# Performance work log

Measured on AMD Instinct MI355X. Metric: run time of the kernel, lower is better.

Reference implementation:

```python
import jax, jax.numpy as jnp
import numpy as np

NUM_HEADS = 16   # matches init_kwargs
WARP_Q = 32      # per-warp Q quant granularity (rows)
BLK_K = 64       # per-block K quant granularity (rows)
EPS = 1e-8


def setup_inputs() -> dict:
    key = jax.random.key(0)
    kq, kk, kv = jax.random.split(key, 3)
    b, s, hid = 2, 2048, 2048
    q = jax.random.normal(kq, (b, s, hid), jnp.float32)
    k = jax.random.normal(kk, (b, s, hid), jnp.float32)
    v = jax.random.normal(kv, (b, s, hid), jnp.float32)
    return {"q": q, "k": k, "v": v, "window_left": 1024, "window_right": 1024}


def _quant_int8(x, group):
    # x: [b, h, s, d] -> int8-valued floats + per-row scales [b, h, s, 1]
    b, h, s, d = x.shape
    xg = x.reshape(b, h, s // group, group, d)
    scale = jnp.maximum(jnp.max(jnp.abs(xg), axis=(3, 4), keepdims=True) / 127.0, EPS)
    xq = jnp.clip(jnp.round(xg / scale), -127.0, 127.0)
    scale_rows = jnp.broadcast_to(scale, (b, h, s // group, group, 1)).reshape(b, h, s, 1)
    return xq.reshape(b, h, s, d), scale_rows


def _sage_attention(q, k, v, window_left, window_right):
    b, s, hid = q.shape
    n = NUM_HEADS
    d = hid // n
    sm_scale = 1.0 / np.sqrt(d)
    # [b, s, n*d] -> [b, n, s, d]
    qh = q.reshape(b, s, n, d).transpose(0, 2, 1, 3)
    kh = k.reshape(b, s, n, d).transpose(0, 2, 1, 3)
    vh = v.reshape(b, s, n, d).transpose(0, 2, 1, 3)

    # smooth K: subtract per-channel seq mean (softmax-invariant)
    k_mean = jnp.mean(kh, axis=2, keepdims=True)
    ks = kh - k_mean

    # per-warp int8 quantization of Q and K
    qq, q_scale = _quant_int8(qh, WARP_Q)
    kq, k_scale = _quant_int8(ks, BLK_K)

    # int8 QK^T, dequantized: [b, n, s, s]
    scores = jnp.einsum('bhid,bhjd->bhij', qq, kq)
    scores = scores * q_scale * jnp.swapaxes(k_scale, -1, -2) * sm_scale

    # sliding window mask (window < 0 means unlimited on that side)
    i = jnp.arange(s)[:, None]
    j = jnp.arange(s)[None, :]
    allowed = jnp.ones((s, s), dtype=bool)
    if window_left >= 0:
        allowed = allowed & ((i - j) <= window_left)
    if window_right >= 0:
        allowed = allowed & ((j - i) <= window_right)
    scores = jnp.where(allowed, scores, -jnp.inf)

    p = jax.nn.softmax(scores, axis=-1)

    # smooth V + fp16 PV accumulation
    v_mean = jnp.mean(vh, axis=2, keepdims=True)
    out16 = jnp.matmul(p.astype(jnp.float16), (vh - v_mean).astype(jnp.float16),
                       preferred_element_type=jnp.float16)
    out = out16.astype(jnp.float32) + v_mean  # rows of p sum to 1

    # [b, n, s, d] -> [b, s, n*d]
    return out.transpose(0, 2, 1, 3).reshape(b, s, n * d)


def reference(q, k, v, window_left, window_right):
    return _sage_attention(q, k, v, window_left, window_right)
```

## Files before the change

### kernel.cpp

```cpp
#include <hip/hip_runtime.h>
#include <hip/hip_fp16.h>
#include <math.h>

#define S_LEN 2048
#define NHID  2048
#define D_HEAD 128
#define N_BH  32
#define EPS_Q 1e-8f

typedef _Float16 half8 __attribute__((ext_vector_type(8)));
typedef _Float16 half4 __attribute__((ext_vector_type(4)));
typedef float floatx4 __attribute__((ext_vector_type(4)));
typedef int int4v __attribute__((ext_vector_type(4)));

__global__ void means_kernel(const float* __restrict__ kk, const float* __restrict__ vv,
                             float* __restrict__ ksumP, float* __restrict__ vsumP) {
  int blk = blockIdx.x;
  int bh = blk >> 5, chunk = blk & 31;
  int b = bh >> 4, h = bh & 15;
  int t = threadIdx.x;
  int d4 = t & 31, sg = t >> 5;
  int s0 = chunk * 64;
  const long base = ((long)(b * S_LEN + s0)) * NHID + h * D_HEAD + d4 * 4;
  floatx4 ks = {0.f,0.f,0.f,0.f}, vs = {0.f,0.f,0.f,0.f};
  #pragma unroll
  for (int j = 0; j < 8; ++j) {
    long idx = base + (long)(sg * 8 + j) * NHID;
    ks += *(const floatx4*)(kk + idx);
    vs += *(const floatx4*)(vv + idx);
  }
  __shared__ floatx4 red[256];
  red[t] = ks; __syncthreads();
  if (t < 128) red[t] += red[t + 128]; __syncthreads();
  if (t < 64)  red[t] += red[t + 64];  __syncthreads();
  if (t < 32) *(floatx4*)(ksumP + (long)blk * 128 + t * 4) = red[t] + red[t + 32];
  __syncthreads();
  red[t] = vs; __syncthreads();
  if (t < 128) red[t] += red[t + 128]; __syncthreads();
  if (t < 64)  red[t] += red[t + 64];  __syncthreads();
  if (t < 32) *(floatx4*)(vsumP + (long)blk * 128 + t * 4) = red[t] + red[t + 32];
}

__global__ void prep_kernel(const float* __restrict__ q, const float* __restrict__ k,
                            const float* __restrict__ v,
                            const float* __restrict__ ksumP, const float* __restrict__ vsumP,
                            signed char* __restrict__ qq, signed char* __restrict__ kq,
                            _Float16* __restrict__ vt,
                            float* __restrict__ qscale, float* __restrict__ kscale,
                            float* __restrict__ vmean) {
  int blk = blockIdx.x;
  int t = threadIdx.x;
  int lane = t & 63, wid = t >> 6;
  __shared__ float wred[4];
  __shared__ __align__(16) _Float16 tile[64 * 136];
  int d4 = t & 31, sg = t >> 5;

  if (blk < 2048) {
    int bh = blk >> 6, g = blk & 63;
    int b = bh >> 4, h = bh & 15;
    int s0 = g * 32;
    const long gbase = ((long)(b * S_LEN + s0)) * NHID + h * D_HEAD + d4 * 4;
    floatx4 vals[4]; float am = 0.f;
    #pragma unroll
    for (int j = 0; j < 4; ++j) {
      floatx4 x = *(const floatx4*)(q + gbase + (long)(sg + j * 8) * NHID);
      vals[j] = x;
      am = fmaxf(am, fmaxf(fmaxf(fabsf(x[0]), fabsf(x[1])), fmaxf(fabsf(x[2]), fabsf(x[3]))));
    }
    #pragma unroll
    for (int off = 1; off < 64; off <<= 1) am = fmaxf(am, __shfl_xor(am, off, 64));
    if (lane == 0) wred[wid] = am;
    __syncthreads();
    am = fmaxf(fmaxf(wred[0], wred[1]), fmaxf(wred[2], wred[3]));
    float scale = fmaxf(am / 127.0f, EPS_Q);
    if (t == 0) qscale[bh * 64 + g] = scale;
    float inv = 1.0f / scale;
    #pragma unroll
    for (int j = 0; j < 4; ++j) {
      int pk = 0;
      #pragma unroll
      for (int c = 0; c < 4; ++c) {
        int qv = (int)fminf(fmaxf(rintf(vals[j][c] * inv), -127.f), 127.f);
        pk |= (qv & 255) << (8 * c);
      }
      ((int*)qq)[((long)bh * S_LEN + s0 + sg + j * 8) * 32 + d4] = pk;
    }
  } else if (blk < 3072) {
    int bb = blk - 2048;
    int bh = bb >> 5, g = bb & 31;
    int b = bh >> 4, h = bh & 15;
    int s0 = g * 64;
    floatx4 msum = {0.f,0.f,0.f,0.f};
    #pragma unroll
    for (int c = 0; c < 32; ++c)
      msum += *(const floatx4*)(ksumP + (long)(bh * 32 + c) * 128 + d4 * 4);
    floatx4 mean = msum * (1.0f / 2048.0f);
    const long gbase = ((long)(b * S_LEN + s0)) * NHID + h * D_HEAD + d4 * 4;
    floatx4 vals[8]; float am = 0.f;
    #pragma unroll
    for (int j = 0; j < 8; ++j) {
      floatx4 x = *(const floatx4*)(k + gbase + (long)(sg + j * 8) * NHID) - mean;
      vals[j] = x;
      am = fmaxf(am, fmaxf(fmaxf(fabsf(x[0]), fabsf(x[1])), fmaxf(fabsf(x[2]), fabsf(x[3]))));
    }
    #pragma unroll
    for (int off = 1; off < 64; off <<= 1) am = fmaxf(am, __shfl_xor(am, off, 64));
    if (lane == 0) wred[wid] = am;
    __syncthreads();
    am = fmaxf(fmaxf(wred[0], wred[1]), fmaxf(wred[2], wred[3]));
    float scale = fmaxf(am / 127.0f, EPS_Q);
    if (t == 0) kscale[bh * 32 + g] = scale;
    float inv = 1.0f / scale;
    #pragma unroll
    for (int j = 0; j < 8; ++j) {
      int pk = 0;
      #pragma unroll
      for (int c = 0; c < 4; ++c) {
        int qv = (int)fminf(fmaxf(rintf(vals[j][c] * inv), -127.f), 127.f);
        pk |= (qv & 255) << (8 * c);
      }
      ((int*)kq)[((long)bh * S_LEN + s0 + sg + j * 8) * 32 + d4] = pk;
    }
  } else {
    int bb = blk - 3072;
    int bh = bb >> 5, st = bb & 31;
    int b = bh >> 4, h = bh & 15;
    int s0 = st * 64;
    floatx4 msum = {0.f,0.f,0.f,0.f};
    #pragma unroll
    for (int c = 0; c < 32; ++c)
      msum += *(const floatx4*)(vsumP + (long)(bh * 32 + c) * 128 + d4 * 4);
    floatx4 mean = msum * (1.0f / 2048.0f);
    if (st == 0 && sg == 0)
      *(floatx4*)(vmean + bh * D_HEAD + d4 * 4) = mean;
    const long gbase = ((long)(b * S_LEN + s0)) * NHID + h * D_HEAD + d4 * 4;
    #pragma unroll
    for (int j = 0; j < 8; ++j) {
      floatx4 x = *(const floatx4*)(v + gbase + (long)(sg + j * 8) * NHID) - mean;
      half4 hv = { (_Float16)x[0], (_Float16)x[1], (_Float16)x[2], (_Float16)x[3] };
      *(half4*)(tile + (sg + j * 8) * 136 + d4 * 4) = hv;
    }
    __syncthreads();
    int dr = t >> 1, sh = (t & 1) * 32;
    _Float16* dst = vt + ((long)bh * D_HEAD + dr) * S_LEN + s0 + sh;
    #pragma unroll
    for (int jo = 0; jo < 4; ++jo) {
      union { half8 v8; _Float16 h[8]; } u;
      #pragma unroll
      for (int ji = 0; ji < 8; ++ji) u.h[ji] = tile[(sh + jo * 8 + ji) * 136 + dr];
      *(half8*)(dst + jo * 8) = u.v8;
    }
  }
}

__launch_bounds__(256, 2)
__global__ void attn_kernel(const signed char* __restrict__ qq, const signed char* __restrict__ kq,
                            const _Float16* __restrict__ vt,
                            const float* __restrict__ qscale, const float* __restrict__ kscale,
                            const float* __restrict__ vmean,
                            const int* __restrict__ wlp, const int* __restrict__ wrp,
                            float* __restrict__ out) {
  int bid = blockIdx.x;
  int xcd = bid & 7, rest = bid >> 3;
  int bh = xcd * 4 + (rest & 3);
  int qb = rest >> 2;
  int b = bh >> 4, h = bh & 15;
  int q0 = qb * 128;

  int wl = *wlp; if (wl < 0) wl = S_LEN;
  int wr = *wrp; if (wr < 0) wr = S_LEN;

  int t = threadIdx.x;
  int wv = t >> 6;
  int lane = t & 63;
  int ln = lane & 15;
  int qd = lane >> 4;

  int r0 = q0 + wv * 32;

  __shared__ __align__(16) signed char Kl[64 * 128];
  __shared__ __align__(16) _Float16 Vl[128 * 64];

  int4v qa8[2][2];
  #pragma unroll
  for (int mh = 0; mh < 2; ++mh) {
    const signed char* qbase = qq + ((long)bh * S_LEN + r0 + mh * 16 + ln) * 128 + qd * 16;
    #pragma unroll
    for (int ks2 = 0; ks2 < 2; ++ks2)
      qa8[mh][ks2] = *(const int4v*)(qbase + ks2 * 64);
  }
  float qs = qscale[bh * 64 + (r0 >> 5)];

  float mrow[2];
  floatx4 lacc[2];
  floatx4 oacc[2][8];
  #pragma unroll
  for (int mh = 0; mh < 2; ++mh) {
    mrow[mh] = -1e30f;
    #pragma unroll
    for (int r = 0; r < 4; ++r) lacc[mh][r] = 0.f;
    #pragma unroll
    for (int nd = 0; nd < 8; ++nd) oacc[mh][nd] = (floatx4){0.f,0.f,0.f,0.f};
  }

  int lo = q0 - wl; if (lo < 0) lo = 0;
  int hi = q0 + 127 + wr; if (hi > S_LEN - 1) hi = S_LEN - 1;
  int t_lo = lo >> 6, t_hi = hi >> 6;

  const float sm_scale2 = 0.08838834764831845f * 1.4426950408889634f;
  const signed char* kbase = kq + (long)bh * S_LEN * 128;
  const _Float16* vbase = vt + (long)bh * D_HEAD * S_LEN;
  const float* kscb = kscale + bh * 32;
  const half8 vones = { (_Float16)1, (_Float16)1, (_Float16)1, (_Float16)1,
                        (_Float16)1, (_Float16)1, (_Float16)1, (_Float16)1 };

  int4v kpre[2];
  half8 vpre[4];
  {
    int j0 = t_lo * 64;
    #pragma unroll
    for (int c = 0; c < 2; ++c) {
      int gc = t + c * 256;
      kpre[c] = *(const int4v*)(kbase + (long)(j0 + (gc >> 3)) * 128 + (gc & 7) * 16);
    }
    #pragma unroll
    for (int c = 0; c < 4; ++c) {
      int gc = t + c * 256;
      vpre[c] = *(const half8*)(vbase + (long)(gc >> 3) * S_LEN + j0 + (gc & 7) * 8);
    }
  }

  for (int tt = t_lo; tt <= t_hi; ++tt) {
    int j0 = tt * 64;
    __syncthreads();
    #pragma unroll
    for (int c = 0; c < 2; ++c) {
      int gc = t + c * 256;
      int row = gc >> 3, ci = gc & 7;
      int cs = (ci ^ row) & 7;
      *(int4v*)(Kl + row * 128 + cs * 16) = kpre[c];
    }
    #pragma unroll
    for (int c = 0; c < 4; ++c) {
      int gc = t + c * 256;
      int row = gc >> 3, ci = gc & 7;
      int cs = (ci ^ row) & 7;
      *(half8*)(Vl + row * 64 + cs * 8) = vpre[c];
    }
    __syncthreads();
    if (tt < t_hi) {
      int j1 = j0 + 64;
      #pragma unroll
      for (int c = 0; c < 2; ++c) {
        int gc = t + c * 256;
        kpre[c] = *(const int4v*)(kbase + (long)(j1 + (gc >> 3)) * 128 + (gc & 7) * 16);
      }
      #pragma unroll
      for (int c = 0; c < 4; ++c) {
        int gc = t + c * 256;
        vpre[c] = *(const half8*)(vbase + (long)(gc >> 3) * S_LEN + j1 + (gc & 7) * 8);
      }
    }

    if (j0 + 63 < r0 - wl || j0 > r0 + 31 + wr) continue;

    float dscale2 = qs * kscb[tt] * sm_scale2;

    int4v isacc[2][4];
    #pragma unroll
    for (int mh = 0; mh < 2; ++mh)
      #pragma unroll
      for (int nb = 0; nb < 4; ++nb) isacc[mh][nb] = (int4v){0,0,0,0};
    #pragma unroll
    for (int nb = 0; nb < 4; ++nb)
      #pragma unroll
      for (int ks2 = 0; ks2 < 2; ++ks2) {
        int ci = ks2 * 4 + qd;
        int cs = (ci ^ ln) & 7;
        int4v kf = *(const int4v*)(Kl + (nb * 16 + ln) * 128 + cs * 16);
        isacc[0][nb] = __builtin_amdgcn_mfma_i32_16x16x64_i8(kf, qa8[0][ks2], isacc[0][nb], 0, 0, 0);
        isacc[1][nb] = __builtin_amdgcn_mfma_i32_16x16x64_i8(kf, qa8[1][ks2], isacc[1][nb], 0, 0, 0);
      }

    half8 pa[2][2];
    #pragma unroll
    for (int mh = 0; mh < 2; ++mh) {
      int rb = r0 + mh * 16;
      bool need_mask = (j0 < rb + 15 - wl) || (j0 + 63 > rb + wr);
      int row = rb + ln;
      int mi[4][4];
      #pragma unroll
      for (int nb = 0; nb < 4; ++nb)
        #pragma unroll
        for (int r = 0; r < 4; ++r) {
          int s = isacc[mh][nb][r];
          if (need_mask) {
            int col = j0 + nb * 16 + qd * 4 + r;
            bool ok = (row - col <= wl) && (col - row <= wr);
            s = ok ? s : -1073741824;
          }
          mi[nb][r] = s;
        }
      int mxi = mi[0][0];
      #pragma unroll
      for (int nb = 0; nb < 4; ++nb)
        #pragma unroll
        for (int r = 0; r < 4; ++r) mxi = (mi[nb][r] > mxi) ? mi[nb][r] : mxi;
      {
        int o = __shfl_xor(mxi, 16, 64); mxi = (o > mxi) ? o : mxi;
        o = __shfl_xor(mxi, 32, 64);     mxi = (o > mxi) ? o : mxi;
      }
      float mx = (float)mxi * dscale2;

      if (__any(mx > mrow[mh] + 11.5f)) {
        float mnew = fmaxf(mrow[mh], mx);
        float alpha = __builtin_amdgcn_exp2f(mrow[mh] - mnew);
        mrow[mh] = mnew;
        float ar[4];
        #pragma unroll
        for (int r = 0; r < 4; ++r) ar[r] = __shfl(alpha, qd * 4 + r, 64);
        #pragma unroll
        for (int nd = 0; nd < 8; ++nd) {
          floatx4 o = oacc[mh][nd];
          #pragma unroll
          for (int r = 0; r < 4; ++r) o[r] *= ar[r];
          oacc[mh][nd] = o;
        }
        #pragma unroll
        for (int r = 0; r < 4; ++r) lacc[mh][r] *= ar[r];
      }

      float m0 = mrow[mh];
      #pragma unroll
      for (int ks = 0; ks < 2; ++ks) {
        half8 tf;
        #pragma unroll
        for (int r = 0; r < 4; ++r) {
          tf[r]     = (_Float16)__builtin_amdgcn_exp2f(fmaf((float)mi[2 * ks][r],     dscale2, -m0));
          tf[4 + r] = (_Float16)__builtin_amdgcn_exp2f(fmaf((float)mi[2 * ks + 1][r], dscale2, -m0));
        }
        pa[mh][ks] = tf;
      }
    }

    #pragma unroll
    for (int nd = 0; nd < 8; ++nd) {
      int rowv = nd * 16 + ln;
      #pragma unroll
      for (int ks = 0; ks < 2; ++ks) {
        int ci0 = ks * 4 + (qd >> 1);
        int o4 = (qd & 1) * 4;
        int cs0 = (ci0 ^ rowv) & 7;
        int cs1 = ((ci0 + 2) ^ rowv) & 7;
        half4 v0 = *(const half4*)(Vl + rowv * 64 + cs0 * 8 + o4);
        half4 v1 = *(const half4*)(Vl + rowv * 64 + cs1 * 8 + o4);
        half8 vf = { v0[0], v0[1], v0[2], v0[3], v1[0], v1[1], v1[2], v1[3] };
        oacc[0][nd] = __builtin_amdgcn_mfma_f32_16x16x32_f16(pa[0][ks], vf, oacc[0][nd], 0, 0, 0);
        oacc[1][nd] = __builtin_amdgcn_mfma_f32_16x16x32_f16(pa[1][ks], vf, oacc[1][nd], 0, 0, 0);
      }
    }
    #pragma unroll
    for (int mh = 0; mh < 2; ++mh) {
      lacc[mh] = __builtin_amdgcn_mfma_f32_16x16x32_f16(pa[mh][0], vones, lacc[mh], 0, 0, 0);
      lacc[mh] = __builtin_amdgcn_mfma_f32_16x16x32_f16(pa[mh][1], vones, lacc[mh], 0, 0, 0);
    }
  }

  float vm[8];
  #pragma unroll
  for (int nd = 0; nd < 8; ++nd)
    vm[nd] = vmean[bh * D_HEAD + nd * 16 + ln];
  float* obase = out + ((long)b * S_LEN) * NHID + h * D_HEAD;
  #pragma unroll
  for (int mh = 0; mh < 2; ++mh)
    #pragma unroll
    for (int r = 0; r < 4; ++r) {
      int row = r0 + mh * 16 + qd * 4 + r;
      float linv = 1.0f / lacc[mh][r];
      #pragma unroll
      for (int nd = 0; nd < 8; ++nd) {
        float o16 = (float)(_Float16)(oacc[mh][nd][r] * linv);
        obase[(long)row * NHID + nd * 16 + ln] = o16 + vm[nd];
      }
    }
}

extern "C" void kernel_launch(void* const* d_in, const int* in_sizes, int n_in,
                              void* d_out, int out_size, void* d_ws, size_t ws_size,
                              hipStream_t stream) {
  (void)in_sizes; (void)n_in; (void)out_size; (void)ws_size;
  const float* q = (const float*)d_in[0];
  const float* k = (const float*)d_in[1];
  const float* v = (const float*)d_in[2];
  const int* wl = (const int*)d_in[3];
  const int* wr = (const int*)d_in[4];
  float* out = (float*)d_out;

  char* ws = (char*)d_ws;
  size_t off = 0;
  const size_t i8sz = (size_t)N_BH * S_LEN * D_HEAD;
  const size_t f16sz = (size_t)N_BH * S_LEN * D_HEAD * sizeof(_Float16);
  signed char* qq = (signed char*)(ws + off); off += i8sz;
  signed char* kq = (signed char*)(ws + off); off += i8sz;
  _Float16* vt = (_Float16*)(ws + off); off += f16sz;
  float* ksumP  = (float*)(ws + off); off += (size_t)N_BH * 32 * 128 * sizeof(float);
  float* vsumP  = (float*)(ws + off); off += (size_t)N_BH * 32 * 128 * sizeof(float);
  float* vmean  = (float*)(ws + off); off += N_BH * D_HEAD * sizeof(float);
  float* qscale = (float*)(ws + off); off += N_BH * 64 * sizeof(float);
  float* kscale = (float*)(ws + off); off += N_BH * 32 * sizeof(float);

  means_kernel<<<1024, 256, 0, stream>>>(k, v, ksumP, vsumP);
  prep_kernel<<<4096, 256, 0, stream>>>(q, k, v, ksumP, vsumP, qq, kq, vt, qscale, kscale, vmean);
  attn_kernel<<<512, 256, 0, stream>>>(qq, kq, vt, qscale, kscale, vmean, wl, wr, out);
}
```

Measured before the change: 223.1 us.

## Move Q quantization into means kernel and permute V transpose for vector loads

Q quantization moves out of the prep kernel into the first kernel alongside the K/V mean reduction, since it does not depend on the means. This shortens the dependent second kernel and balances the two launches. The V transpose writes keys in a permuted order so each lane's 8 fp16 B-operand values sit contiguously in shared memory. The attention loop can then fetch them with one half8 load instead of two half4 loads. Correctness depends on the permutation matching the key order used by the P fragment.

Result: no change. 221.3 us (-0.8%).

```diff
diff --git a/kernel.cpp b/kernel.cpp
--- a/kernel.cpp
+++ b/kernel.cpp
@@ -13,41 +13,76 @@
 typedef float floatx4 __attribute__((ext_vector_type(4)));
 typedef int int4v __attribute__((ext_vector_type(4)));
 
-__global__ void means_kernel(const float* __restrict__ kk, const float* __restrict__ vv,
-                             float* __restrict__ ksumP, float* __restrict__ vsumP) {
+__global__ void mq_kernel(const float* __restrict__ kk, const float* __restrict__ vv,
+                          const float* __restrict__ q,
+                          float* __restrict__ ksumP, float* __restrict__ vsumP,
+                          signed char* __restrict__ qq, float* __restrict__ qscale) {
   int blk = blockIdx.x;
-  int bh = blk >> 5, chunk = blk & 31;
-  int b = bh >> 4, h = bh & 15;
   int t = threadIdx.x;
   int d4 = t & 31, sg = t >> 5;
-  int s0 = chunk * 64;
-  const long base = ((long)(b * S_LEN + s0)) * NHID + h * D_HEAD + d4 * 4;
-  floatx4 ks = {0.f,0.f,0.f,0.f}, vs = {0.f,0.f,0.f,0.f};
-  #pragma unroll
-  for (int j = 0; j < 8; ++j) {
-    long idx = base + (long)(sg * 8 + j) * NHID;
-    ks += *(const floatx4*)(kk + idx);
-    vs += *(const floatx4*)(vv + idx);
-  }
   __shared__ floatx4 red[256];
-  red[t] = ks; __syncthreads();
-  if (t < 128) red[t] += red[t + 128]; __syncthreads();
-  if (t < 64)  red[t] += red[t + 64];  __syncthreads();
-  if (t < 32) *(floatx4*)(ksumP + (long)blk * 128 + t * 4) = red[t] + red[t + 32];
-  __syncthreads();
-  red[t] = vs; __syncthreads();
-  if (t < 128) red[t] += red[t + 128]; __syncthreads();
-  if (t < 64)  red[t] += red[t + 64];  __syncthreads();
-  if (t < 32) *(floatx4*)(vsumP + (long)blk * 128 + t * 4) = red[t] + red[t + 32];
+  __shared__ float wred[4];
+
+  if (blk < 1024) {
+    int bh = blk >> 5, chunk = blk & 31;
+    int b = bh >> 4, h = bh & 15;
+    int s0 = chunk * 64;
+    const long base = ((long)(b * S_LEN + s0)) * NHID + h * D_HEAD + d4 * 4;
+    floatx4 ks = {0.f,0.f,0.f,0.f}, vs = {0.f,0.f,0.f,0.f};
+    #pragma unroll
+    for (int j = 0; j < 8; ++j) {
+      long idx = base + (long)(sg * 8 + j) * NHID;
+      ks += *(const floatx4*)(kk + idx);
+      vs += *(const floatx4*)(vv + idx);
+    }
+    red[t] = ks; __syncthreads();
+    if (t < 128) red[t] += red[t + 128]; __syncthreads();
+    if (t < 64)  red[t] += red[t + 64];  __syncthreads();
+    if (t < 32) *(floatx4*)(ksumP + (long)blk * 128 + t * 4) = red[t] + red[t + 32];
+    __syncthreads();
+    red[t] = vs; __syncthreads();
+    if (t < 128) red[t] += red[t + 128]; __syncthreads();
+    if (t < 64)  red[t] += red[t + 64];  __syncthreads();
+    if (t < 32) *(floatx4*)(vsumP + (long)blk * 128 + t * 4) = red[t] + red[t + 32];
+  } else {
+    int bb = blk - 1024;
+    int bh = bb >> 6, g = bb & 63;
+    int b = bh >> 4, h = bh & 15;
+    int s0 = g * 32;
+    int lane = t & 63, wid = t >> 6;
+    const long gbase = ((long)(b * S_LEN + s0)) * NHID + h * D_HEAD + d4 * 4;
+    floatx4 vals[4]; float am = 0.f;
+    #pragma unroll
+    for (int j = 0; j < 4; ++j) {
+      floatx4 x = *(const floatx4*)(q + gbase + (long)(sg + j * 8) * NHID);
+      vals[j] = x;
+      am = fmaxf(am, fmaxf(fmaxf(fabsf(x[0]), fabsf(x[1])), fmaxf(fabsf(x[2]), fabsf(x[3]))));
+    }
+    #pragma unroll
+    for (int off = 1; off < 64; off <<= 1) am = fmaxf(am, __shfl_xor(am, off, 64));
+    if (lane == 0) wred[wid] = am;
+    __syncthreads();
+    am = fmaxf(fmaxf(wred[0], wred[1]), fmaxf(wred[2], wred[3]));
+    float scale = fmaxf(am / 127.0f, EPS_Q);
+    if (t == 0) qscale[bh * 64 + g] = scale;
+    float inv = 1.0f / scale;
+    #pragma unroll
+    for (int j = 0; j < 4; ++j) {
+      int pk = 0;
+      #pragma unroll
+      for (int c = 0; c < 4; ++c) {
+        int qv = (int)fminf(fmaxf(rintf(vals[j][c] * inv), -127.f), 127.f);
+        pk |= (qv & 255) << (8 * c);
+      }
+      ((int*)qq)[((long)bh * S_LEN + s0 + sg + j * 8) * 32 + d4] = pk;
+    }
+  }
 }
 
-__global__ void prep_kernel(const float* __restrict__ q, const float* __restrict__ k,
-                            const float* __restrict__ v,
-                            const float* __restrict__ ksumP, const float* __restrict__ vsumP,
-                            signed char* __restrict__ qq, signed char* __restrict__ kq,
-                            _Float16* __restrict__ vt,
-                            float* __restrict__ qscale, float* __restrict__ kscale,
-                            float* __restrict__ vmean) {
+__global__ void kv_kernel(const float* __restrict__ k, const float* __restrict__ v,
+                          const float* __restrict__ ksumP, const float* __restrict__ vsumP,
+                          signed char* __restrict__ kq, _Float16* __restrict__ vt,
+                          float* __restrict__ kscale, float* __restrict__ vmean) {
   int blk = blockIdx.x;
   int t = threadIdx.x;
   int lane = t & 63, wid = t >> 6;
@@ -55,39 +90,8 @@
   __shared__ __align__(16) _Float16 tile[64 * 136];
   int d4 = t & 31, sg = t >> 5;
 
-  if (blk < 2048) {
-    int bh = blk >> 6, g = blk & 63;
-    int b = bh >> 4, h = bh & 15;
-    int s0 = g * 32;
-    const long gbase = ((long)(b * S_LEN + s0)) * NHID + h * D_HEAD + d4 * 4;
-    floatx4 vals[4]; float am = 0.f;
-    #pragma unroll
-    for (int j = 0; j < 4; ++j) {
-      floatx4 x = *(const floatx4*)(q + gbase + (long)(sg + j * 8) * NHID);
-      vals[j] = x;
-      am = fmaxf(am, fmaxf(fmaxf(fabsf(x[0]), fabsf(x[1])), fmaxf(fabsf(x[2]), fabsf(x[3]))));
-    }
-    #pragma unroll
-    for (int off = 1; off < 64; off <<= 1) am = fmaxf(am, __shfl_xor(am, off, 64));
-    if (lane == 0) wred[wid] = am;
-    __syncthreads();
-    am = fmaxf(fmaxf(wred[0], wred[1]), fmaxf(wred[2], wred[3]));
-    float scale = fmaxf(am / 127.0f, EPS_Q);
-    if (t == 0) qscale[bh * 64 + g] = scale;
-    float inv = 1.0f / scale;
-    #pragma unroll
-    for (int j = 0; j < 4; ++j) {
-      int pk = 0;
-      #pragma unroll
-      for (int c = 0; c < 4; ++c) {
-        int qv = (int)fminf(fmaxf(rintf(vals[j][c] * inv), -127.f), 127.f);
-        pk |= (qv & 255) << (8 * c);
-      }
-      ((int*)qq)[((long)bh * S_LEN + s0 + sg + j * 8) * 32 + d4] = pk;
-    }
-  } else if (blk < 3072) {
-    int bb = blk - 2048;
-    int bh = bb >> 5, g = bb & 31;
+  if (blk < 1024) {
+    int bh = blk >> 5, g = blk & 31;
     int b = bh >> 4, h = bh & 15;
     int s0 = g * 64;
     floatx4 msum = {0.f,0.f,0.f,0.f};
@@ -122,7 +126,7 @@
       ((int*)kq)[((long)bh * S_LEN + s0 + sg + j * 8) * 32 + d4] = pk;
     }
   } else {
-    int bb = blk - 3072;
+    int bb = blk - 1024;
     int bh = bb >> 5, st = bb & 31;
     int b = bh >> 4, h = bh & 15;
     int s0 = st * 64;
@@ -147,7 +151,10 @@
     for (int jo = 0; jo < 4; ++jo) {
       union { half8 v8; _Float16 h[8]; } u;
       #pragma unroll
-      for (int ji = 0; ji < 8; ++ji) u.h[ji] = tile[(sh + jo * 8 + ji) * 136 + dr];
+      for (int ji = 0; ji < 8; ++ji) {
+        int key = jo * 4 + ji + (ji >= 4 ? 12 : 0);
+        u.h[ji] = tile[(sh + key) * 136 + dr];
+      }
       *(half8*)(dst + jo * 8) = u.v8;
     }
   }
@@ -348,13 +355,9 @@
       int rowv = nd * 16 + ln;
       #pragma unroll
       for (int ks = 0; ks < 2; ++ks) {
-        int ci0 = ks * 4 + (qd >> 1);
-        int o4 = (qd & 1) * 4;
-        int cs0 = (ci0 ^ rowv) & 7;
-        int cs1 = ((ci0 + 2) ^ rowv) & 7;
-        half4 v0 = *(const half4*)(Vl + rowv * 64 + cs0 * 8 + o4);
-        half4 v1 = *(const half4*)(Vl + rowv * 64 + cs1 * 8 + o4);
-        half8 vf = { v0[0], v0[1], v0[2], v0[3], v1[0], v1[1], v1[2], v1[3] };
+        int ci = ks * 4 + qd;
+        int cs = (ci ^ rowv) & 7;
+        half8 vf = *(const half8*)(Vl + rowv * 64 + cs * 8);
         oacc[0][nd] = __builtin_amdgcn_mfma_f32_16x16x32_f16(pa[0][ks], vf, oacc[0][nd], 0, 0, 0);
         oacc[1][nd] = __builtin_amdgcn_mfma_f32_16x16x32_f16(pa[1][ks], vf, oacc[1][nd], 0, 0, 0);
       }
@@ -409,7 +412,7 @@
   float* qscale = (float*)(ws + off); off += N_BH * 64 * sizeof(float);
   float* kscale = (float*)(ws + off); off += N_BH * 32 * sizeof(float);
 
-  means_kernel<<<1024, 256, 0, stream>>>(k, v, ksumP, vsumP);
-  prep_kernel<<<4096, 256, 0, stream>>>(q, k, v, ksumP, vsumP, qq, kq, vt, qscale, kscale, vmean);
+  mq_kernel<<<3072, 256, 0, stream>>>(k, v, q, ksumP, vsumP, qq, qscale);
+  kv_kernel<<<2048, 256, 0, stream>>>(k, v, ksumP, vsumP, kq, vt, kscale, vmean);
   attn_kernel<<<512, 256, 0, stream>>>(qq, kq, vt, qscale, kscale, vmean, wl, wr, out);
 }
```
